# Kernel optimization log

Measured on AMD Instinct MI355X. Metric: run time of the kernel, lower is better.

The kernel has to match this reference:

```python
import jax, jax.numpy as jnp
import numpy as np

SR = 16000; HOP = 160; NM = 80; FMIN = 80.0; FMAX = 8000.0
T = 4 * SR              # 64000 samples
NSTAGE = 4              # cascaded biquad stages per channel
D = 256; NH = 8; DH = 32; NL = 8; DFF = 1024
BN_EPS = 1e-5; LN_EPS = 1e-5


def _biquad_coeffs():
    fc = np.logspace(np.log10(FMIN), np.log10(FMAX), NM)           # [NM]
    q = 4.0 + 2.0 * np.arange(NSTAGE)                               # [4]
    omega = 2.0 * np.pi * fc / SR
    alpha = np.sin(omega)[None, :] / (2.0 * q[:, None])             # [4,NM]
    a0 = 1.0 + alpha
    b0 = alpha / a0
    b2 = -alpha / a0
    a1 = (-2.0 * np.cos(omega))[None, :] / a0
    a2 = (1.0 - alpha) / a0
    return tuple(jnp.asarray(c, jnp.float32) for c in (b0, b2, a1, a2))


def _cochlear(x):
    # x: [B,T] -> [B,NM,T]; 4-stage cascaded bandpass biquads, zero initial state.
    b0, b2, a1, a2 = _biquad_coeffs()
    B = x.shape[0]
    z = jnp.zeros((NSTAGE, NM, B), x.dtype)

    def body(carry, xt):
        x1, x2, y1, y2 = carry                      # each [4,NM,B]
        sig = jnp.broadcast_to(xt[None, :], (NM, B))
        nx1, nx2, ny1, ny2 = [], [], [], []
        for s in range(NSTAGE):                     # fixed small cascade
            y = (b0[s][:, None] * sig + b2[s][:, None] * x2[s]
                 - a1[s][:, None] * y1[s] - a2[s][:, None] * y2[s])
            nx1.append(sig); nx2.append(x1[s]); ny1.append(y); ny2.append(y1[s])
            sig = y
        return (jnp.stack(nx1), jnp.stack(nx2), jnp.stack(ny1), jnp.stack(ny2)), sig

    _, ys = jax.lax.scan(body, (z, z, z, z), x.T)   # ys: [T,NM,B]
    return ys.transpose(2, 1, 0)


def _ln(x, g, b):
    m = x.mean(-1, keepdims=True)
    v = jnp.mean((x - m) ** 2, -1, keepdims=True)
    return (x - m) * jax.lax.rsqrt(v + LN_EPS) * g + b


def _cbr(h, w, b, g, bb):
    h = jax.lax.conv_general_dilated(h, w, (1, 1), 'SAME',
                                     dimension_numbers=('NCHW', 'OIHW', 'NCHW'))
    h = h + b[None, :, None, None]
    # eval-mode BatchNorm2d: running_mean=0, running_var=1
    h = h * (g / np.sqrt(1.0 + BN_EPS))[None, :, None, None] + bb[None, :, None, None]
    return jax.nn.relu(h)


def _mha(x, wqkv, bqkv, wo, bo):
    B, S, _ = x.shape
    qkv = x @ wqkv.T + bqkv
    q, k, v = jnp.split(qkv, 3, axis=-1)
    heads = lambda t: t.reshape(B, S, NH, DH).transpose(0, 2, 1, 3)
    q, k, v = heads(q), heads(k), heads(v)
    attn = jax.nn.softmax(jnp.einsum('bhqd,bhkd->bhqk', q, k) / np.sqrt(DH), axis=-1)
    o = jnp.einsum('bhqk,bhkd->bhqd', attn, v).transpose(0, 2, 1, 3).reshape(B, S, D)
    return o @ wo.T + bo


def _forward(x, cw1, cb1, g1, be1, cw2, cb2, g2, be2, cw3, cb3, g3, be3,
             qkv_w, qkv_b, out_w, out_b, ln1_g, ln1_b,
             ff1_w, ff1_b, ff2_w, ff2_b, ln2_g, ln2_b, pw, pb):
    B = x.shape[0]
    sig = _cochlear(x)                                    # [B,80,T]
    env = jnp.abs(sig)
    frames = env.reshape(B, NM, T // HOP, HOP).mean(-1)   # avg_pool1d k=s=160 -> [B,80,400]
    feats = jnp.log(frames + 1e-8)[:, None]               # [B,1,80,400]
    h = _cbr(feats, cw1, cb1, g1, be1)
    h = _cbr(h, cw2, cb2, g2, be2)
    h = _cbr(h, cw3, cb3, g3, be3)                        # [B,256,80,400]
    # AdaptiveAvgPool2d((80,32)): H already 80 (identity); pool W 400->32 with torch bin rule
    W_in, W_out = h.shape[-1], 32
    bins = [(int(np.floor(i * W_in / W_out)), int(np.ceil((i + 1) * W_in / W_out)))
            for i in range(W_out)]
    h = jnp.stack([h[..., s:e].mean(-1) for s, e in bins], axis=-1)   # [B,256,80,32]
    tok = h.reshape(B, D, -1).transpose(0, 2, 1)          # [B,2560,256]
    for l in range(NL):   # post-norm encoder layer, relu FFN, dropout=0 (eval)
        a = _mha(tok, qkv_w[l], qkv_b[l], out_w[l], out_b[l])
        tok = _ln(tok + a, ln1_g[l], ln1_b[l])
        f = jax.nn.relu(tok @ ff1_w[l].T + ff1_b[l]) @ ff2_w[l].T + ff2_b[l]
        tok = _ln(tok + f, ln2_g[l], ln2_b[l])
    return tok @ pw.T + pb                                # [B,2560,512]


def setup_inputs() -> dict:
    key = jax.random.key(0)
    ks = jax.random.split(key, 16)
    w = lambda k, shape, std=0.02: jax.random.normal(k, shape, jnp.float32) * std
    return {
        'x': jax.random.normal(ks[0], (1, T), jnp.float32),
        'cw1': w(ks[1], (64, 1, 3, 3), 0.1), 'cb1': jnp.zeros((64,)),
        'g1': jnp.ones((64,)), 'be1': jnp.zeros((64,)),
        'cw2': w(ks[2], (128, 64, 3, 3), 0.05), 'cb2': jnp.zeros((128,)),
        'g2': jnp.ones((128,)), 'be2': jnp.zeros((128,)),
        'cw3': w(ks[3], (256, 128, 3, 3), 0.05), 'cb3': jnp.zeros((256,)),
        'g3': jnp.ones((256,)), 'be3': jnp.zeros((256,)),
        'qkv_w': w(ks[4], (NL, 3 * D, D)), 'qkv_b': jnp.zeros((NL, 3 * D)),
        'out_w': w(ks[5], (NL, D, D)), 'out_b': jnp.zeros((NL, D)),
        'ln1_g': jnp.ones((NL, D)), 'ln1_b': jnp.zeros((NL, D)),
        'ff1_w': w(ks[6], (NL, DFF, D)), 'ff1_b': jnp.zeros((NL, DFF)),
        'ff2_w': w(ks[7], (NL, D, DFF)), 'ff2_b': jnp.zeros((NL, D)),
        'ln2_g': jnp.ones((NL, D)), 'ln2_b': jnp.zeros((NL, D)),
        'pw': w(ks[8], (512, D)), 'pb': jnp.zeros((512,)),
    }


def reference(x, cw1, cb1, g1, be1, cw2, cb2, g2, be2, cw3, cb3, g3, be3,
              qkv_w, qkv_b, out_w, out_b, ln1_g, ln1_b,
              ff1_w, ff1_b, ff2_w, ff2_b, ln2_g, ln2_b, pw, pb):
    return _forward(x, cw1, cb1, g1, be1, cw2, cb2, g2, be2, cw3, cb3, g3, be3,
                    qkv_w, qkv_b, out_w, out_b, ln1_g, ln1_b,
                    ff1_w, ff1_b, ff2_w, ff2_b, ln2_g, ln2_b, pw, pb)
```

## Files before the change

### kernel.cpp

```cpp
#include <hip/hip_runtime.h>
#include <hip/hip_bf16.h>
#include <math.h>

typedef __hip_bfloat16 bf16;
typedef short s16x8 __attribute__((ext_vector_type(8)));
typedef float f32x4 __attribute__((ext_vector_type(4)));

__device__ __forceinline__ float b2f(const bf16 v) { return __bfloat162float(v); }
__device__ __forceinline__ float ldf(int isbf, const void* p, size_t i) {
    return isbf ? __bfloat162float(((const bf16*)p)[i]) : ((const float*)p)[i];
}
__device__ __forceinline__ double ldd(int isbf, const void* p, size_t i) {
    return (double)ldf(isbf, p, i);
}
__device__ __forceinline__ short sbf(float f) {
    bf16 h = __float2bfloat16(f);
    return *(short*)&h;
}
__device__ __forceinline__ s16x8 cvt8(float4 a, float4 b) {
    union { bf16 h[8]; s16x8 v; } u;
    u.h[0] = __float2bfloat16(a.x); u.h[1] = __float2bfloat16(a.y);
    u.h[2] = __float2bfloat16(a.z); u.h[3] = __float2bfloat16(a.w);
    u.h[4] = __float2bfloat16(b.x); u.h[5] = __float2bfloat16(b.y);
    u.h[6] = __float2bfloat16(b.z); u.h[7] = __float2bfloat16(b.w);
    return u.v;
}

#define TLEN   64000
#define NMEL   80
#define CHUNK  160
#define NCHK   400
#define SEQ    2560
#define DMODEL 256
#define PI_D   3.14159265358979323846
#define CLW    420

#define F_COEF  0ul
#define F_FLAG  2560ul
#define F_M     2576ul
#define F_V     12816ul
#define F_INI   524816ul
#define F_FEATS 1036816ul
#define F_TOK   1068816ul
#define F_BIG   1724176ul
#define O_C1CL  0ul
#define O_C2CL  1102080ul
#define O_C3    3306240ul
#define O_WTB2  11500000ul
#define O_WTB3  11540000ul

__global__ void k_detect(const unsigned short* __restrict__ g, int* __restrict__ flag) {
    if (threadIdx.x == 0 && blockIdx.x == 0) *flag = (g[0] == 0x3F80) ? 1 : 0;
}

__global__ void k_coeffs(double* __restrict__ cf) {
    int i = blockIdx.x * 256 + threadIdx.x;
    if (i >= 4 * NMEL) return;
    int s = i / NMEL, m = i % NMEL;
    double lg0 = log10(80.0), lg1 = log10(8000.0);
    double fc = pow(10.0, lg0 + (lg1 - lg0) * (double)m / 79.0);
    double q = 4.0 + 2.0 * (double)s;
    double omega = 2.0 * PI_D * fc / 16000.0;
    double al = sin(omega) / (2.0 * q);
    double a0 = 1.0 + al;
    cf[i * 4 + 0] = (double)(float)(al / a0);
    cf[i * 4 + 1] = (double)(float)(-al / a0);
    cf[i * 4 + 2] = (double)(float)(-2.0 * cos(omega) / a0);
    cf[i * 4 + 3] = (double)(float)((1.0 - al) / a0);
}

__global__ __launch_bounds__(256) void k_bqf_zero(const void* __restrict__ x,
        const double* __restrict__ cf, const int* __restrict__ flagp,
        double* __restrict__ v) {
    int i = blockIdx.x * 256 + threadIdx.x;
    if (i >= NMEL * NCHK) return;
    int isbf = *flagp;
    int j = i / NMEL, m = i % NMEL;
    double b0[4], b2[4], a1[4], a2[4];
#pragma unroll
    for (int s = 0; s < 4; ++s) {
        const double* c = &cf[(s * NMEL + m) * 4];
        b0[s] = c[0]; b2[s] = c[1]; a1[s] = c[2]; a2[s] = c[3];
    }
    int t0 = j * CHUNK;
    double x1 = (t0 > 0) ? ldd(isbf, x, t0 - 1) : 0.0;
    double x2 = (t0 > 1) ? ldd(isbf, x, t0 - 2) : 0.0;
    double s0 = 0, s1 = 0, s2 = 0, s3 = 0, s4 = 0, s5 = 0, s6 = 0, s7 = 0;
    for (int t = t0; t < t0 + CHUNK; ++t) {
        double xt = ldd(isbf, x, t);
        double y0 = fma(b0[0], xt, fma(b2[0], x2, fma(-a1[0], s0, -a2[0] * s1)));
        double y1 = fma(b0[1], y0, fma(b2[1], s1, fma(-a1[1], s2, -a2[1] * s3)));
        double y2 = fma(b0[2], y1, fma(b2[2], s3, fma(-a1[2], s4, -a2[2] * s5)));
        double y3 = fma(b0[3], y2, fma(b2[3], s5, fma(-a1[3], s6, -a2[3] * s7)));
        s1 = s0; s0 = y0; s3 = s2; s2 = y1; s5 = s4; s4 = y2; s7 = s6; s6 = y3;
        x2 = x1; x1 = xt;
    }
    double* vp = &v[((size_t)m * NCHK + j) * 8];
    vp[0] = s0; vp[1] = s1; vp[2] = s2; vp[3] = s3;
    vp[4] = s4; vp[5] = s5; vp[6] = s6; vp[7] = s7;
}

__global__ __launch_bounds__(256) void k_bqA(const double* __restrict__ cf,
                                             double* __restrict__ M) {
    __shared__ double P[4][8][8], R[4][8][8], T[4][8][8];
    int t = threadIdx.x;
    int cg = t >> 6, e8 = t & 63;
    int i = e8 >> 3, jj = e8 & 7;
    int m = blockIdx.x * 4 + cg;
    double b0[4], b2[4], a1[4], a2[4];
#pragma unroll
    for (int s = 0; s < 4; ++s) {
        const double* c = &cf[(s * NMEL + m) * 4];
        b0[s] = c[0]; b2[s] = c[1]; a1[s] = c[2]; a2[s] = c[3];
    }
    double s[8];
#pragma unroll
    for (int k = 0; k < 8; ++k) s[k] = (k == jj) ? 1.0 : 0.0;
    double y0 = fma(-a1[0], s[0], -a2[0] * s[1]);
    double y1 = fma(b0[1], y0, fma(b2[1], s[1], fma(-a1[1], s[2], -a2[1] * s[3])));
    double y2 = fma(b0[2], y1, fma(b2[2], s[3], fma(-a1[2], s[4], -a2[2] * s[5])));
    double y3 = fma(b0[3], y2, fma(b2[3], s[5], fma(-a1[3], s[6], -a2[3] * s[7])));
    double colv[8] = {y0, s[0], y1, s[2], y2, s[4], y3, s[6]};
    P[cg][i][jj] = colv[i];
    R[cg][i][jj] = (i == jj) ? 1.0 : 0.0;
    __syncthreads();
    int e = CHUNK;
    while (e) {
        double acc = 0.0;
#pragma unroll
        for (int k = 0; k < 8; ++k) acc = fma(R[cg][i][k], P[cg][k][jj], acc);
        T[cg][i][jj] = acc;
        __syncthreads();
        if (e & 1) R[cg][i][jj] = T[cg][i][jj];
        __syncthreads();
        acc = 0.0;
#pragma unroll
        for (int k = 0; k < 8; ++k) acc = fma(P[cg][i][k], P[cg][k][jj], acc);
        T[cg][i][jj] = acc;
        __syncthreads();
        P[cg][i][jj] = T[cg][i][jj];
        e >>= 1;
        __syncthreads();
    }
    M[(size_t)m * 64 + i * 8 + jj] = R[cg][i][jj];
}

__global__ __launch_bounds__(512) void k_bq_scan8p(const double* __restrict__ Mbuf,
        const double* __restrict__ v, double* __restrict__ ini) {
    __shared__ double Mp[9][64];
    __shared__ double bufA[NCHK][8];
    __shared__ double bufB[NCHK][8];
    int m = blockIdx.x, t = threadIdx.x;
    if (t < 64) Mp[0][t] = Mbuf[(size_t)m * 64 + t];
    __syncthreads();
    for (int s = 1; s < 9; ++s) {
        if (t < 64) {
            int i = t >> 3, jj = t & 7;
            double acc = 0.0;
#pragma unroll
            for (int k = 0; k < 8; ++k) acc = fma(Mp[s - 1][i * 8 + k], Mp[s - 1][k * 8 + jj], acc);
            Mp[s][t] = acc;
        }
        __syncthreads();
    }
    double b[8];
    if (t < NCHK) {
        const double* vp = &v[((size_t)m * NCHK + t) * 8];
#pragma unroll
        for (int i = 0; i < 8; ++i) { b[i] = vp[i]; bufA[t][i] = b[i]; }
    }
    __syncthreads();
#pragma unroll
    for (int s = 0; s < 9; ++s) {
        int off = 1 << s;
        double nb[8];
        if (t < NCHK) {
            if (t >= off) {
                const double* src = (s & 1) ? bufB[t - off] : bufA[t - off];
#pragma unroll
                for (int i = 0; i < 8; ++i) {
                    double acc = b[i];
#pragma unroll
                    for (int k = 0; k < 8; ++k) acc = fma(Mp[s][i * 8 + k], src[k], acc);
                    nb[i] = acc;
                }
            } else {
#pragma unroll
                for (int i = 0; i < 8; ++i) nb[i] = b[i];
            }
        }
        __syncthreads();
        if (t < NCHK) {
            double* dst = (s & 1) ? bufA[t] : bufB[t];
#pragma unroll
            for (int i = 0; i < 8; ++i) { dst[i] = nb[i]; b[i] = nb[i]; }
        }
        __syncthreads();
    }
    if (t < NCHK) {
        double* op = &ini[((size_t)m * NCHK + t) * 8];
        if (t == 0) {
#pragma unroll
            for (int i = 0; i < 8; ++i) op[i] = 0.0;
        } else {
#pragma unroll
            for (int i = 0; i < 8; ++i) op[i] = bufB[t - 1][i];
        }
    }
}

__global__ __launch_bounds__(256) void k_bqf_emit(const void* __restrict__ x,
        const double* __restrict__ cf, const int* __restrict__ flagp,
        const double* __restrict__ ini, float* __restrict__ feats) {
    int i = blockIdx.x * 256 + threadIdx.x;
    if (i >= NMEL * NCHK) return;
    int isbf = *flagp;
    int j = i / NMEL, m = i % NMEL;
    double b0[4], b2[4], a1[4], a2[4];
#pragma unroll
    for (int s = 0; s < 4; ++s) {
        const double* c = &cf[(s * NMEL + m) * 4];
        b0[s] = c[0]; b2[s] = c[1]; a1[s] = c[2]; a2[s] = c[3];
    }
    int t0 = j * CHUNK;
    double x1 = (t0 > 0) ? ldd(isbf, x, t0 - 1) : 0.0;
    double x2 = (t0 > 1) ? ldd(isbf, x, t0 - 2) : 0.0;
    const double* ip = &ini[((size_t)m * NCHK + j) * 8];
    double s0 = ip[0], s1 = ip[1], s2 = ip[2], s3 = ip[3];
    double s4 = ip[4], s5 = ip[5], s6 = ip[6], s7 = ip[7];
    double acc = 0.0;
    for (int t = t0; t < t0 + CHUNK; ++t) {
        double xt = ldd(isbf, x, t);
        double y0 = fma(b0[0], xt, fma(b2[0], x2, fma(-a1[0], s0, -a2[0] * s1)));
        double y1 = fma(b0[1], y0, fma(b2[1], s1, fma(-a1[1], s2, -a2[1] * s3)));
        double y2 = fma(b0[2], y1, fma(b2[2], s3, fma(-a1[2], s4, -a2[2] * s5)));
        double y3 = fma(b0[3], y2, fma(b2[3], s5, fma(-a1[3], s6, -a2[3] * s7)));
        acc += fabs(y3);
        s1 = s0; s0 = y0; s3 = s2; s2 = y1; s5 = s4; s4 = y2; s7 = s6; s6 = y3;
        x2 = x1; x1 = xt;
    }
    feats[(size_t)m * 400 + j] = (float)log(acc * (1.0 / 160.0) + 1e-8);
}

__global__ void k_fill0(bf16* __restrict__ p, int n8) {
    int i = blockIdx.x * 256 + threadIdx.x;
    if (i < n8) { s16x8 z = {}; ((s16x8*)p)[i] = z; }
}

__global__ void k_wtb(const void* __restrict__ w, const int* __restrict__ flagp,
                      bf16* __restrict__ out, int CO, int CIN) {
    int i = blockIdx.x * 256 + threadIdx.x;
    int K = CIN * 9;
    if (i >= CO * K) return;
    int co = i / K, rem = i % K;
    int c = rem / 288, tp = (rem / 32) % 9, cin = rem & 31;
    out[i] = __float2bfloat16(ldf(*flagp, w, ((size_t)co * CIN + c * 32 + cin) * 9 + tp));
}

__global__ __launch_bounds__(256) void k_conv1cl(const float* __restrict__ in,
        const void* __restrict__ wt, const void* __restrict__ bi,
        const void* __restrict__ ga, const void* __restrict__ be,
        const int* __restrict__ flagp, bf16* __restrict__ out) {
    __shared__ float wsh[576];
    __shared__ float ash[64];
    __shared__ float bsh[64];
    int t = threadIdx.x;
    int isbf = *flagp;
    for (int i = t; i < 576; i += 256) wsh[i] = ldf(isbf, wt, i);
    if (t < 64) {
        float A = ldf(isbf, ga, t) * 0.999995000037f;
        ash[t] = A;
        bsh[t] = fmaf(ldf(isbf, bi, t), A, ldf(isbf, be, t));
    }
    __syncthreads();
    int i = blockIdx.x * 256 + t;
    if (i >= 32000) return;
    int h = i / 400, w = i % 400;
    float xs[9];
#pragma unroll
    for (int dy = 0; dy < 3; ++dy)
#pragma unroll
        for (int dx = 0; dx < 3; ++dx) {
            int hh = h + dy - 1, ww = w + dx - 1;
            xs[dy * 3 + dx] = (hh >= 0 && hh < 80 && ww >= 0 && ww < 400)
                              ? in[hh * 400 + ww] : 0.f;
        }
    bf16* op = out + ((size_t)(h + 1) * CLW + (w + 1)) * 64;
#pragma unroll
    for (int g = 0; g < 8; ++g) {
        union { bf16 h8[8]; s16x8 v; } u;
#pragma unroll
        for (int e = 0; e < 8; ++e) {
            int co = g * 8 + e;
            float acc = 0.f;
#pragma unroll
            for (int uu = 0; uu < 9; ++uu) acc = fmaf(wsh[co * 9 + uu], xs[uu], acc);
            u.h8[e] = __float2bfloat16(fmaxf(fmaf(acc, ash[co], bsh[co]), 0.f));
        }
        *(s16x8*)&op[g * 8] = u.v;
    }
}

template<int CIN, int CO, int CLOUT>
__global__ __launch_bounds__(256) void k_convm(const bf16* __restrict__ cl,
        const bf16* __restrict__ Wtb,
        const void* __restrict__ bi, const void* __restrict__ ga,
        const void* __restrict__ be, const int* __restrict__ flagp,
        void* __restrict__ out) {
    const int MT = CO / 64;
    const int K = CIN * 9;
    __shared__ short Bs[3][36][40];
    int t = threadIdx.x, wv = t >> 6, L = t & 63, quad = L >> 4, lx = L & 15;
    int w0 = blockIdx.x * 32, h = blockIdx.y;
    int cob = wv * (CO / 4);
    f32x4 acc[MT][2] = {};
    for (int c = 0; c < CIN / 32; ++c) {
        __syncthreads();
        for (int u = t; u < 408; u += 256) {
            int seg = u >> 2, part = u & 3;
            int dy = seg / 34, ww = seg % 34;
            *(s16x8*)&Bs[dy][ww][part * 8] =
                *(const s16x8*)&cl[((size_t)(h + dy) * CLW + (w0 + ww)) * CIN + c * 32 + part * 8];
        }
        __syncthreads();
#pragma unroll
        for (int tp = 0; tp < 9; ++tp) {
            int dy = tp / 3, dx = tp % 3;
            int kbase = (c * 9 + tp) * 32;
            s16x8 af[MT];
#pragma unroll
            for (int mt = 0; mt < MT; ++mt)
                af[mt] = *(const s16x8*)&Wtb[(size_t)(cob + mt * 16 + lx) * K + kbase + quad * 8];
#pragma unroll
            for (int n = 0; n < 2; ++n) {
                s16x8 bfr = *(const s16x8*)&Bs[dy][n * 16 + lx + dx][quad * 8];
#pragma unroll
                for (int mt = 0; mt < MT; ++mt)
                    acc[mt][n] = __builtin_amdgcn_mfma_f32_16x16x32_bf16(af[mt], bfr, acc[mt][n], 0, 0, 0);
            }
        }
    }
    int isbf = *flagp;
#pragma unroll
    for (int mt = 0; mt < MT; ++mt) {
#pragma unroll
        for (int r = 0; r < 4; ++r) {
            int co = cob + mt * 16 + quad * 4 + r;
            float A = ldf(isbf, ga, co) * 0.999995000037f;
            float B = fmaf(ldf(isbf, bi, co), A, ldf(isbf, be, co));
#pragma unroll
            for (int n = 0; n < 2; ++n) {
                int w = w0 + n * 16 + lx;
                if (w < 400) {
                    float v = fmaxf(fmaf(acc[mt][n][r], A, B), 0.f);
                    if (CLOUT)
                        ((bf16*)out)[((size_t)(h + 1) * CLW + (w + 1)) * CO + co] = __float2bfloat16(v);
                    else
                        ((float*)out)[(size_t)co * 32000 + h * 400 + w] = v;
                }
            }
        }
    }
}

__global__ __launch_bounds__(256) void k_pool(const float* __restrict__ c3,
                                              float* __restrict__ tok) {
    int i = blockIdx.x * 256 + threadIdx.x;
    if (i >= SEQ * DMODEL) return;
    int s = i >> 8, c = i & 255;
    int f = s >> 5, jj = s & 31;
    int w0 = (jj * 25) >> 1;
    const float* p = c3 + ((size_t)c * 80 + f) * 400 + w0;
    float sum = 0.f;
#pragma unroll
    for (int k = 0; k < 13; ++k) sum += p[k];
    tok[i] = sum * (1.f / 13.f);
}

template<int RELU, int OUTMODE, int NT, int ACOMB>
__global__ __launch_bounds__(256) void k_gemm(const float* __restrict__ A,
        const void* __restrict__ W, size_t woff,
        const void* __restrict__ bias, size_t boff,
        const int* __restrict__ flagp, void* __restrict__ Cout_,
        bf16* __restrict__ vtb, const float* __restrict__ partb,
        int M, int N, int K) {
    __shared__ short As[64][136];
    __shared__ short Bs[NT * 16][136];
    const int isbf = *flagp;
    int t = threadIdx.x;
    int wv = t >> 6, L = t & 63, quad = L >> 4, lx = L & 15;
    int row0 = blockIdx.y * 64, col0 = blockIdx.x * (NT * 16);
    f32x4 acc[NT] = {};
    for (int k0 = 0; k0 < K; k0 += 128) {
        __syncthreads();
        {
            int row = t >> 2, cb = (t & 3) * 8;
#pragma unroll
            for (int c = 0; c < 4; ++c) {
                int col = cb + c * 32;
                s16x8 av;
                if (ACOMB) {
                    int q = row0 + row;
                    int kk = k0 + col;
                    int hh = kk >> 5, d = kk & 31;
                    const float* pa = partb + ((size_t)(hh * 2) * SEQ + q) * 36;
                    const float* pc = pa + (size_t)SEQ * 36;
                    float m0 = pa[32], l0 = pa[33], m1 = pc[32], l1 = pc[33];
                    float Mx = fmaxf(m0, m1);
                    float e0 = __expf(m0 - Mx), e1 = __expf(m1 - Mx);
                    float inv = 1.f / (l0 * e0 + l1 * e1);
                    float4 u0 = *(const float4*)(pa + d), u1 = *(const float4*)(pa + d + 4);
                    float4 v0 = *(const float4*)(pc + d), v1 = *(const float4*)(pc + d + 4);
                    float4 r0, r1;
                    r0.x = (u0.x * e0 + v0.x * e1) * inv; r0.y = (u0.y * e0 + v0.y * e1) * inv;
                    r0.z = (u0.z * e0 + v0.z * e1) * inv; r0.w = (u0.w * e0 + v0.w * e1) * inv;
                    r1.x = (u1.x * e0 + v1.x * e1) * inv; r1.y = (u1.y * e0 + v1.y * e1) * inv;
                    r1.z = (u1.z * e0 + v1.z * e1) * inv; r1.w = (u1.w * e0 + v1.w * e1) * inv;
                    av = cvt8(r0, r1);
                } else {
                    const float* ap = &A[(size_t)(row0 + row) * K + k0 + col];
                    av = cvt8(*(const float4*)ap, *(const float4*)(ap + 4));
                }
                *(s16x8*)&As[row][col] = av;
            }
        }
        if (NT == 4) {
            int row = t >> 2, cb = (t & 3) * 8;
#pragma unroll
            for (int c = 0; c < 4; ++c) {
                int col = cb + c * 32;
                size_t widx = woff + (size_t)(col0 + row) * K + k0 + col;
                s16x8 wv8;
                if (isbf) {
                    wv8 = *(const s16x8*)((const bf16*)W + widx);
                } else {
                    const float* wf = (const float*)W + widx;
                    wv8 = cvt8(*(const float4*)wf, *(const float4*)(wf + 4));
                }
                *(s16x8*)&Bs[row][col] = wv8;
            }
        } else {
            int row = t >> 3, cb = (t & 7) * 8;
#pragma unroll
            for (int c = 0; c < 2; ++c) {
                int col = cb + c * 64;
                size_t widx = woff + (size_t)(col0 + row) * K + k0 + col;
                s16x8 wv8;
                if (isbf) {
                    wv8 = *(const s16x8*)((const bf16*)W + widx);
                } else {
                    const float* wf = (const float*)W + widx;
                    wv8 = cvt8(*(const float4*)wf, *(const float4*)(wf + 4));
                }
                *(s16x8*)&Bs[row][col] = wv8;
            }
        }
        __syncthreads();
#pragma unroll
        for (int kc = 0; kc < 4; ++kc) {
            s16x8 af = *(const s16x8*)&As[wv * 16 + lx][kc * 32 + quad * 8];
#pragma unroll
            for (int n = 0; n < NT; ++n) {
                s16x8 bf_ = *(const s16x8*)&Bs[n * 16 + lx][kc * 32 + quad * 8];
                acc[n] = __builtin_amdgcn_mfma_f32_16x16x32_bf16(af, bf_, acc[n], 0, 0, 0);
            }
        }
    }
#pragma unroll
    for (int n = 0; n < NT; ++n) {
        int col = col0 + n * 16 + lx;
        float bv = ldf(isbf, bias, boff + col);
#pragma unroll
        for (int r = 0; r < 4; ++r) {
            int row = row0 + wv * 16 + quad * 4 + r;
            float val = acc[n][r] + bv;
            if (RELU) val = fmaxf(val, 0.f);
            if (OUTMODE == 0) {
                ((float*)Cout_)[(size_t)row * N + col] = val;
            } else if (OUTMODE == 2) {
                bf16 bb_ = __float2bfloat16(val);
                ((bf16*)Cout_)[(size_t)row * N + col] = bb_;
                if (col >= 512) vtb[(size_t)(col - 512) * SEQ + row] = bb_;
            } else {
                if (isbf) ((bf16*)Cout_)[(size_t)row * N + col] = __float2bfloat16(val);
                else      ((float*)Cout_)[(size_t)row * N + col] = val;
            }
        }
    }
}

__global__ __launch_bounds__(256) void k_flash(const bf16* __restrict__ qkvB,
        const bf16* __restrict__ vtb, float* __restrict__ part) {
    int b = blockIdx.x;
    int pp = b & 1, qb = (b >> 1) % 40, h = b / 80;
    int t = threadIdx.x, wv = t >> 6, L = t & 63, quad = L >> 4, lx = L & 15;
    int q0 = qb * 64;
    __shared__ short Qs[64][40];
    __shared__ short Ks[64][40];
    __shared__ short Vt[32][72];
    __shared__ short Ps[64][72];
    const float scale = 0.17677669529663687f;
    int sr = t >> 2, sk = (t & 3) * 8;
    *(s16x8*)&Qs[sr][sk] = *(const s16x8*)&qkvB[(size_t)(q0 + sr) * 768 + h * 32 + sk];
    f32x4 o[2] = {};
    float mrow[4], lrow[4];
#pragma unroll
    for (int r = 0; r < 4; ++r) { mrow[r] = -INFINITY; lrow[r] = 0.f; }
    int kstart = pp * 1280;
    int vd = t >> 3, vk = (t & 7) * 8;
    for (int kt = 0; kt < 20; ++kt) {
        int kb = kstart + kt * 64;
        __syncthreads();
        *(s16x8*)&Ks[sr][sk] = *(const s16x8*)&qkvB[(size_t)(kb + sr) * 768 + 256 + h * 32 + sk];
        *(s16x8*)&Vt[vd][vk] = *(const s16x8*)&vtb[(size_t)(h * 32 + vd) * SEQ + kb + vk];
        __syncthreads();
        s16x8 qf = *(const s16x8*)&Qs[wv * 16 + lx][quad * 8];
        f32x4 sc[4] = {};
#pragma unroll
        for (int n = 0; n < 4; ++n) {
            s16x8 kf = *(const s16x8*)&Ks[n * 16 + lx][quad * 8];
            sc[n] = __builtin_amdgcn_mfma_f32_16x16x32_bf16(qf, kf, sc[n], 0, 0, 0);
        }
#pragma unroll
        for (int r = 0; r < 4; ++r) {
            float tm = -INFINITY;
#pragma unroll
            for (int n = 0; n < 4; ++n) { sc[n][r] *= scale; tm = fmaxf(tm, sc[n][r]); }
#pragma unroll
            for (int mk = 1; mk < 16; mk <<= 1) tm = fmaxf(tm, __shfl_xor(tm, mk));
            float mn = fmaxf(mrow[r], tm);
            float al = __expf(mrow[r] - mn);
            float ps = 0.f;
#pragma unroll
            for (int n = 0; n < 4; ++n) {
                float e = __expf(sc[n][r] - mn);
                sc[n][r] = e; ps += e;
            }
#pragma unroll
            for (int mk = 1; mk < 16; mk <<= 1) ps += __shfl_xor(ps, mk);
            lrow[r] = lrow[r] * al + ps;
            mrow[r] = mn;
            o[0][r] *= al; o[1][r] *= al;
            int qrow = wv * 16 + quad * 4 + r;
#pragma unroll
            for (int n = 0; n < 4; ++n) Ps[qrow][n * 16 + lx] = sbf(sc[n][r]);
        }
        __syncthreads();
#pragma unroll
        for (int ks = 0; ks < 2; ++ks) {
            s16x8 pf = *(const s16x8*)&Ps[wv * 16 + lx][ks * 32 + quad * 8];
#pragma unroll
            for (int n = 0; n < 2; ++n) {
                s16x8 vf = *(const s16x8*)&Vt[n * 16 + lx][ks * 32 + quad * 8];
                o[n] = __builtin_amdgcn_mfma_f32_16x16x32_bf16(pf, vf, o[n], 0, 0, 0);
            }
        }
    }
#pragma unroll
    for (int r = 0; r < 4; ++r) {
        int q = q0 + wv * 16 + quad * 4 + r;
        size_t pb_ = ((size_t)(h * 2 + pp) * SEQ + q) * 36;
        part[pb_ + lx] = o[0][r];
        part[pb_ + 16 + lx] = o[1][r];
        if (lx == 0) { part[pb_ + 32] = mrow[r]; part[pb_ + 33] = lrow[r]; }
    }
}

__global__ __launch_bounds__(256) void k_ln(float* __restrict__ tok,
        const float* __restrict__ res, const void* __restrict__ gg,
        const void* __restrict__ bb, size_t goff, const int* __restrict__ flagp) {
    int isbf = *flagp;
    int row = blockIdx.x * 4 + (threadIdx.x >> 6);
    int lane = threadIdx.x & 63;
    float* tp = tok + (size_t)row * DMODEL;
    const float* rp = res + (size_t)row * DMODEL;
    float4 a = *(const float4*)&tp[lane * 4];
    float4 r = *(const float4*)&rp[lane * 4];
    float x0 = a.x + r.x, x1 = a.y + r.y, x2 = a.z + r.z, x3 = a.w + r.w;
    float s = x0 + x1 + x2 + x3;
#pragma unroll
    for (int mk = 1; mk < 64; mk <<= 1) s += __shfl_xor(s, mk);
    float mean = s * (1.f / 256.f);
    float d0 = x0 - mean, d1 = x1 - mean, d2 = x2 - mean, d3 = x3 - mean;
    float vs = d0 * d0 + d1 * d1 + d2 * d2 + d3 * d3;
#pragma unroll
    for (int mk = 1; mk < 64; mk <<= 1) vs += __shfl_xor(vs, mk);
    float rstd = rsqrtf(vs * (1.f / 256.f) + 1e-5f);
    size_t c = goff + lane * 4;
    float y0 = fmaf(d0 * rstd, ldf(isbf, gg, c + 0), ldf(isbf, bb, c + 0));
    float y1 = fmaf(d1 * rstd, ldf(isbf, gg, c + 1), ldf(isbf, bb, c + 1));
    float y2 = fmaf(d2 * rstd, ldf(isbf, gg, c + 2), ldf(isbf, bb, c + 2));
    float y3 = fmaf(d3 * rstd, ldf(isbf, gg, c + 3), ldf(isbf, bb, c + 3));
    *(float4*)&tp[lane * 4] = make_float4(y0, y1, y2, y3);
}

extern "C" void kernel_launch(void* const* d_in, const int* in_sizes, int n_in,
                              void* d_out, int out_size, void* d_ws, size_t ws_size,
                              hipStream_t stream) {
    const void* x    = d_in[0];
    const void* cw1  = d_in[1];  const void* cb1 = d_in[2];
    const void* g1   = d_in[3];  const void* be1 = d_in[4];
    const void* cw2  = d_in[5];  const void* cb2 = d_in[6];
    const void* g2   = d_in[7];  const void* be2 = d_in[8];
    const void* cw3  = d_in[9];  const void* cb3 = d_in[10];
    const void* g3   = d_in[11]; const void* be3 = d_in[12];
    const void* qkvw = d_in[13]; const void* qkvb = d_in[14];
    const void* outw = d_in[15]; const void* outb = d_in[16];
    const void* ln1g = d_in[17]; const void* ln1b = d_in[18];
    const void* ff1w = d_in[19]; const void* ff1b = d_in[20];
    const void* ff2w = d_in[21]; const void* ff2b = d_in[22];
    const void* ln2g = d_in[23]; const void* ln2b = d_in[24];
    const void* pw   = d_in[25]; const void* pb   = d_in[26];

    float*  ws    = (float*)d_ws;
    double* coef  = (double*)(ws + F_COEF);
    int*    flagp = (int*)(ws + F_FLAG);
    double* Mbuf  = (double*)(ws + F_M);
    double* vbuf  = (double*)(ws + F_V);
    double* ini   = (double*)(ws + F_INI);
    float*  feats = ws + F_FEATS;
    float*  tok   = ws + F_TOK;
    bf16*   c1cl  = (bf16*)(ws + F_BIG + O_C1CL);
    bf16*   c2cl  = (bf16*)(ws + F_BIG + O_C2CL);
    float*  c3    = ws + F_BIG + O_C3;
    bf16*   Wtb2  = (bf16*)(ws + F_BIG + O_WTB2);
    bf16*   Wtb3  = (bf16*)(ws + F_BIG + O_WTB3);
    bf16*   qkvB  = (bf16*)(ws + F_BIG);
    bf16*   vtb   = (bf16*)(ws + F_BIG + 983040ul);
    float*  partb = ws + F_BIG + 1310720ul;
    float*  proj  = ws + F_BIG + 2785280ul;
    float*  ff1bf = ws + F_BIG + 3440640ul;

    k_detect<<<dim3(1), dim3(64), 0, stream>>>((const unsigned short*)ln1g, flagp);
    k_coeffs<<<dim3(2), dim3(256), 0, stream>>>(coef);
    k_wtb<<<dim3(288), dim3(256), 0, stream>>>(cw2, flagp, Wtb2, 128, 64);
    k_wtb<<<dim3(1152), dim3(256), 0, stream>>>(cw3, flagp, Wtb3, 256, 128);

    k_bqA<<<dim3(20), dim3(256), 0, stream>>>(coef, Mbuf);
    k_bqf_zero<<<dim3(125), dim3(256), 0, stream>>>(x, coef, flagp, vbuf);
    k_bq_scan8p<<<dim3(80), dim3(512), 0, stream>>>(Mbuf, vbuf, ini);
    k_bqf_emit<<<dim3(125), dim3(256), 0, stream>>>(x, coef, flagp, ini, feats);

    k_fill0<<<dim3(1077), dim3(256), 0, stream>>>(c1cl, 275520);
    k_fill0<<<dim3(2153), dim3(256), 0, stream>>>(c2cl, 551040);
    k_conv1cl<<<dim3(125), dim3(256), 0, stream>>>(feats, cw1, cb1, g1, be1, flagp, c1cl);
    k_convm<64, 128, 1><<<dim3(13, 80), dim3(256), 0, stream>>>(
        c1cl, Wtb2, cb2, g2, be2, flagp, c2cl);
    k_convm<128, 256, 0><<<dim3(13, 80), dim3(256), 0, stream>>>(
        c2cl, Wtb3, cb3, g3, be3, flagp, c3);

    k_pool<<<dim3(2560), dim3(256), 0, stream>>>(c3, tok);

    for (int l = 0; l < 8; ++l) {
        k_gemm<0, 2, 4, 0><<<dim3(12, 40), dim3(256), 0, stream>>>(
            tok, qkvw, (size_t)l * 768 * 256, qkvb, (size_t)l * 768,
            flagp, qkvB, vtb, nullptr, SEQ, 768, 256);
        k_flash<<<dim3(640), dim3(256), 0, stream>>>(qkvB, vtb, partb);
        k_gemm<0, 0, 2, 1><<<dim3(8, 40), dim3(256), 0, stream>>>(
            nullptr, outw, (size_t)l * 256 * 256, outb, (size_t)l * 256,
            flagp, proj, nullptr, partb, SEQ, 256, 256);
        k_ln<<<dim3(640), dim3(256), 0, stream>>>(tok, proj, ln1g, ln1b, (size_t)l * 256, flagp);
        k_gemm<1, 0, 4, 0><<<dim3(16, 40), dim3(256), 0, stream>>>(
            tok, ff1w, (size_t)l * 1024 * 256, ff1b, (size_t)l * 1024,
            flagp, ff1bf, nullptr, nullptr, SEQ, 1024, 256);
        k_gemm<0, 0, 2, 0><<<dim3(8, 40), dim3(256), 0, stream>>>(
            ff1bf, ff2w, (size_t)l * 256 * 1024, ff2b, (size_t)l * 256,
            flagp, proj, nullptr, nullptr, SEQ, 256, 1024);
        k_ln<<<dim3(640), dim3(256), 0, stream>>>(tok, proj, ln2g, ln2b, (size_t)l * 256, flagp);
    }

    k_gemm<0, 1, 2, 0><<<dim3(16, 40), dim3(256), 0, stream>>>(
        tok, pw, 0ul, pb, 0ul, flagp, d_out, nullptr, nullptr, SEQ, 512, 256);
}
```

Baseline: 1.273 ms.

## Fuse out-proj and FF2 GEMMs with residual LayerNorm; tile conv over two rows

Adds a full-row GEMM kernel (64 rows x 256 cols per block) that adds bias and residual and applies LayerNorm in the epilogue. It replaces the out-projection and FF2 GEMMs plus their separate LN kernels, which removes the proj round trip and two launches per layer. FF1 output now goes out as bf16 and FF2 reads it directly. The conv MFMA kernel also computes two output rows per block, reusing weight fragments and halving the grid. The trade-off is that the fused GEMM launches only 40 blocks, which may leave many CUs idle.

```diff
diff --git a/kernel.cpp b/kernel.cpp
--- a/kernel.cpp
+++ b/kernel.cpp
@@ -309,18 +309,18 @@
         void* __restrict__ out) {
     const int MT = CO / 64;
     const int K = CIN * 9;
-    __shared__ short Bs[3][36][40];
+    __shared__ short Bs[4][36][40];
     int t = threadIdx.x, wv = t >> 6, L = t & 63, quad = L >> 4, lx = L & 15;
-    int w0 = blockIdx.x * 32, h = blockIdx.y;
+    int w0 = blockIdx.x * 32, h0 = blockIdx.y * 2;
     int cob = wv * (CO / 4);
-    f32x4 acc[MT][2] = {};
+    f32x4 acc[MT][2][2] = {};
     for (int c = 0; c < CIN / 32; ++c) {
         __syncthreads();
-        for (int u = t; u < 408; u += 256) {
+        for (int u = t; u < 544; u += 256) {
             int seg = u >> 2, part = u & 3;
             int dy = seg / 34, ww = seg % 34;
             *(s16x8*)&Bs[dy][ww][part * 8] =
-                *(const s16x8*)&cl[((size_t)(h + dy) * CLW + (w0 + ww)) * CIN + c * 32 + part * 8];
+                *(const s16x8*)&cl[((size_t)(h0 + dy) * CLW + (w0 + ww)) * CIN + c * 32 + part * 8];
         }
         __syncthreads();
 #pragma unroll
@@ -332,11 +332,14 @@
             for (int mt = 0; mt < MT; ++mt)
                 af[mt] = *(const s16x8*)&Wtb[(size_t)(cob + mt * 16 + lx) * K + kbase + quad * 8];
 #pragma unroll
-            for (int n = 0; n < 2; ++n) {
-                s16x8 bfr = *(const s16x8*)&Bs[dy][n * 16 + lx + dx][quad * 8];
-#pragma unroll
-                for (int mt = 0; mt < MT; ++mt)
-                    acc[mt][n] = __builtin_amdgcn_mfma_f32_16x16x32_bf16(af[mt], bfr, acc[mt][n], 0, 0, 0);
+            for (int hr = 0; hr < 2; ++hr) {
+#pragma unroll
+                for (int n = 0; n < 2; ++n) {
+                    s16x8 bfr = *(const s16x8*)&Bs[dy + hr][n * 16 + lx + dx][quad * 8];
+#pragma unroll
+                    for (int mt = 0; mt < MT; ++mt)
+                        acc[mt][hr][n] = __builtin_amdgcn_mfma_f32_16x16x32_bf16(af[mt], bfr, acc[mt][hr][n], 0, 0, 0);
+                }
             }
         }
     }
@@ -349,14 +352,18 @@
             float A = ldf(isbf, ga, co) * 0.999995000037f;
             float B = fmaf(ldf(isbf, bi, co), A, ldf(isbf, be, co));
 #pragma unroll
-            for (int n = 0; n < 2; ++n) {
-                int w = w0 + n * 16 + lx;
-                if (w < 400) {
-                    float v = fmaxf(fmaf(acc[mt][n][r], A, B), 0.f);
-                    if (CLOUT)
-                        ((bf16*)out)[((size_t)(h + 1) * CLW + (w + 1)) * CO + co] = __float2bfloat16(v);
-                    else
-                        ((float*)out)[(size_t)co * 32000 + h * 400 + w] = v;
+            for (int hr = 0; hr < 2; ++hr) {
+                int h = h0 + hr;
+#pragma unroll
+                for (int n = 0; n < 2; ++n) {
+                    int w = w0 + n * 16 + lx;
+                    if (w < 400) {
+                        float v = fmaxf(fmaf(acc[mt][hr][n][r], A, B), 0.f);
+                        if (CLOUT)
+                            ((bf16*)out)[((size_t)(h + 1) * CLW + (w + 1)) * CO + co] = __float2bfloat16(v);
+                        else
+                            ((float*)out)[(size_t)co * 32000 + h * 400 + w] = v;
+                    }
                 }
             }
         }
@@ -481,10 +488,117 @@
                 bf16 bb_ = __float2bfloat16(val);
                 ((bf16*)Cout_)[(size_t)row * N + col] = bb_;
                 if (col >= 512) vtb[(size_t)(col - 512) * SEQ + row] = bb_;
+            } else if (OUTMODE == 3) {
+                ((bf16*)Cout_)[(size_t)row * N + col] = __float2bfloat16(val);
             } else {
                 if (isbf) ((bf16*)Cout_)[(size_t)row * N + col] = __float2bfloat16(val);
                 else      ((float*)Cout_)[(size_t)row * N + col] = val;
             }
+        }
+    }
+}
+
+template<int ABF16, int ACOMB>
+__global__ __launch_bounds__(256) void k_gemmln(const void* __restrict__ A,
+        const void* __restrict__ W, size_t woff,
+        const void* __restrict__ bias, size_t boff,
+        const void* __restrict__ gg, const void* __restrict__ bb, size_t goff,
+        const int* __restrict__ flagp, float* __restrict__ tok,
+        const float* __restrict__ partb, int K) {
+    __shared__ short As[64][72];
+    __shared__ short Bs[256][72];
+    const int isbf = *flagp;
+    int t = threadIdx.x;
+    int wv = t >> 6, L = t & 63, quad = L >> 4, lx = L & 15;
+    int row0 = blockIdx.x * 64;
+    f32x4 acc[16] = {};
+    for (int k0 = 0; k0 < K; k0 += 64) {
+        __syncthreads();
+        {
+            int row = t >> 2, cb = (t & 3) * 16;
+#pragma unroll
+            for (int c = 0; c < 2; ++c) {
+                int col = cb + c * 8;
+                s16x8 av;
+                if (ACOMB) {
+                    int q = row0 + row;
+                    int kk = k0 + col;
+                    int hh = kk >> 5, d = kk & 31;
+                    const float* pa = partb + ((size_t)(hh * 2) * SEQ + q) * 36;
+                    const float* pc = pa + (size_t)SEQ * 36;
+                    float m0 = pa[32], l0 = pa[33], m1 = pc[32], l1 = pc[33];
+                    float Mx = fmaxf(m0, m1);
+                    float e0 = __expf(m0 - Mx), e1 = __expf(m1 - Mx);
+                    float inv = 1.f / (l0 * e0 + l1 * e1);
+                    float4 u0 = *(const float4*)(pa + d), u1 = *(const float4*)(pa + d + 4);
+                    float4 v0 = *(const float4*)(pc + d), v1 = *(const float4*)(pc + d + 4);
+                    float4 r0, r1;
+                    r0.x = (u0.x * e0 + v0.x * e1) * inv; r0.y = (u0.y * e0 + v0.y * e1) * inv;
+                    r0.z = (u0.z * e0 + v0.z * e1) * inv; r0.w = (u0.w * e0 + v0.w * e1) * inv;
+                    r1.x = (u1.x * e0 + v1.x * e1) * inv; r1.y = (u1.y * e0 + v1.y * e1) * inv;
+                    r1.z = (u1.z * e0 + v1.z * e1) * inv; r1.w = (u1.w * e0 + v1.w * e1) * inv;
+                    av = cvt8(r0, r1);
+                } else if (ABF16) {
+                    av = *(const s16x8*)((const bf16*)A + (size_t)(row0 + row) * K + k0 + col);
+                } else {
+                    const float* ap = (const float*)A + (size_t)(row0 + row) * K + k0 + col;
+                    av = cvt8(*(const float4*)ap, *(const float4*)(ap + 4));
+                }
+                *(s16x8*)&As[row][col] = av;
+            }
+        }
+        {
+#pragma unroll
+            for (int c = 0; c < 8; ++c) {
+                int col = c * 8;
+                size_t widx = woff + (size_t)t * K + k0 + col;
+                s16x8 wv8;
+                if (isbf) {
+                    wv8 = *(const s16x8*)((const bf16*)W + widx);
+                } else {
+                    const float* wf = (const float*)W + widx;
+                    wv8 = cvt8(*(const float4*)wf, *(const float4*)(wf + 4));
+                }
+                *(s16x8*)&Bs[t][col] = wv8;
+            }
+        }
+        __syncthreads();
+#pragma unroll
+        for (int kc = 0; kc < 2; ++kc) {
+            s16x8 af = *(const s16x8*)&As[wv * 16 + lx][kc * 32 + quad * 8];
+#pragma unroll
+            for (int n = 0; n < 16; ++n) {
+                s16x8 bf_ = *(const s16x8*)&Bs[n * 16 + lx][kc * 32 + quad * 8];
+                acc[n] = __builtin_amdgcn_mfma_f32_16x16x32_bf16(af, bf_, acc[n], 0, 0, 0);
+            }
+        }
+    }
+#pragma unroll
+    for (int r = 0; r < 4; ++r) {
+        int row = row0 + wv * 16 + quad * 4 + r;
+        float* tp = tok + (size_t)row * DMODEL;
+        float vals[16];
+        float s = 0.f;
+#pragma unroll
+        for (int n = 0; n < 16; ++n) {
+            int col = n * 16 + lx;
+            float v = acc[n][r] + ldf(isbf, bias, boff + col) + tp[col];
+            vals[n] = v; s += v;
+        }
+#pragma unroll
+        for (int mk = 1; mk < 16; mk <<= 1) s += __shfl_xor(s, mk);
+        float mean = s * (1.f / 256.f);
+        float vs = 0.f;
+#pragma unroll
+        for (int n = 0; n < 16; ++n) { float d = vals[n] - mean; vs += d * d; }
+#pragma unroll
+        for (int mk = 1; mk < 16; mk <<= 1) vs += __shfl_xor(vs, mk);
+        float rstd = rsqrtf(vs * (1.f / 256.f) + 1e-5f);
+#pragma unroll
+        for (int n = 0; n < 16; ++n) {
+            int col = n * 16 + lx;
+            tp[col] = fmaf((vals[n] - mean) * rstd, ldf(isbf, gg, goff + col),
+                           ldf(isbf, bb, goff + col));
         }
     }
 }
@@ -564,34 +678,6 @@
         part[pb_ + 16 + lx] = o[1][r];
         if (lx == 0) { part[pb_ + 32] = mrow[r]; part[pb_ + 33] = lrow[r]; }
     }
-}
-
-__global__ __launch_bounds__(256) void k_ln(float* __restrict__ tok,
-        const float* __restrict__ res, const void* __restrict__ gg,
-        const void* __restrict__ bb, size_t goff, const int* __restrict__ flagp) {
-    int isbf = *flagp;
-    int row = blockIdx.x * 4 + (threadIdx.x >> 6);
-    int lane = threadIdx.x & 63;
-    float* tp = tok + (size_t)row * DMODEL;
-    const float* rp = res + (size_t)row * DMODEL;
-    float4 a = *(const float4*)&tp[lane * 4];
-    float4 r = *(const float4*)&rp[lane * 4];
-    float x0 = a.x + r.x, x1 = a.y + r.y, x2 = a.z + r.z, x3 = a.w + r.w;
-    float s = x0 + x1 + x2 + x3;
-#pragma unroll
-    for (int mk = 1; mk < 64; mk <<= 1) s += __shfl_xor(s, mk);
-    float mean = s * (1.f / 256.f);
-    float d0 = x0 - mean, d1 = x1 - mean, d2 = x2 - mean, d3 = x3 - mean;
-    float vs = d0 * d0 + d1 * d1 + d2 * d2 + d3 * d3;
-#pragma unroll
-    for (int mk = 1; mk < 64; mk <<= 1) vs += __shfl_xor(vs, mk);
-    float rstd = rsqrtf(vs * (1.f / 256.f) + 1e-5f);
-    size_t c = goff + lane * 4;
-    float y0 = fmaf(d0 * rstd, ldf(isbf, gg, c + 0), ldf(isbf, bb, c + 0));
-    float y1 = fmaf(d1 * rstd, ldf(isbf, gg, c + 1), ldf(isbf, bb, c + 1));
-    float y2 = fmaf(d2 * rstd, ldf(isbf, gg, c + 2), ldf(isbf, bb, c + 2));
-    float y3 = fmaf(d3 * rstd, ldf(isbf, gg, c + 3), ldf(isbf, bb, c + 3));
-    *(float4*)&tp[lane * 4] = make_float4(y0, y1, y2, y3);
 }
 
 extern "C" void kernel_launch(void* const* d_in, const int* in_sizes, int n_in,
@@ -628,8 +714,7 @@
     bf16*   qkvB  = (bf16*)(ws + F_BIG);
     bf16*   vtb   = (bf16*)(ws + F_BIG + 983040ul);
     float*  partb = ws + F_BIG + 1310720ul;
-    float*  proj  = ws + F_BIG + 2785280ul;
-    float*  ff1bf = ws + F_BIG + 3440640ul;
+    bf16*   ff1bf = (bf16*)(ws + F_BIG + 2785280ul);
 
     k_detect<<<dim3(1), dim3(64), 0, stream>>>((const unsigned short*)ln1g, flagp);
     k_coeffs<<<dim3(2), dim3(256), 0, stream>>>(coef);
@@ -644,9 +729,9 @@
     k_fill0<<<dim3(1077), dim3(256), 0, stream>>>(c1cl, 275520);
     k_fill0<<<dim3(2153), dim3(256), 0, stream>>>(c2cl, 551040);
     k_conv1cl<<<dim3(125), dim3(256), 0, stream>>>(feats, cw1, cb1, g1, be1, flagp, c1cl);
-    k_convm<64, 128, 1><<<dim3(13, 80), dim3(256), 0, stream>>>(
+    k_convm<64, 128, 1><<<dim3(13, 40), dim3(256), 0, stream>>>(
         c1cl, Wtb2, cb2, g2, be2, flagp, c2cl);
-    k_convm<128, 256, 0><<<dim3(13, 80), dim3(256), 0, stream>>>(
+    k_convm<128, 256, 0><<<dim3(13, 40), dim3(256), 0, stream>>>(
         c2cl, Wtb3, cb3, g3, be3, flagp, c3);
 
     k_pool<<<dim3(2560), dim3(256), 0, stream>>>(c3, tok);
@@ -656,17 +741,15 @@
             tok, qkvw, (size_t)l * 768 * 256, qkvb, (size_t)l * 768,
             flagp, qkvB, vtb, nullptr, SEQ, 768, 256);
         k_flash<<<dim3(640), dim3(256), 0, stream>>>(qkvB, vtb, partb);
-        k_gemm<0, 0, 2, 1><<<dim3(8, 40), dim3(256), 0, stream>>>(
+        k_gemmln<0, 1><<<dim3(40), dim3(256), 0, stream>>>(
             nullptr, outw, (size_t)l * 256 * 256, outb, (size_t)l * 256,
-            flagp, proj, nullptr, partb, SEQ, 256, 256);
-        k_ln<<<dim3(640), dim3(256), 0, stream>>>(tok, proj, ln1g, ln1b, (size_t)l * 256, flagp);
-        k_gemm<1, 0, 4, 0><<<dim3(16, 40), dim3(256), 0, stream>>>(
+            ln1g, ln1b, (size_t)l * 256, flagp, tok, partb, 256);
+        k_gemm<1, 3, 4, 0><<<dim3(16, 40), dim3(256), 0, stream>>>(
             tok, ff1w, (size_t)l * 1024 * 256, ff1b, (size_t)l * 1024,
             flagp, ff1bf, nullptr, nullptr, SEQ, 1024, 256);
-        k_gemm<0, 0, 2, 0><<<dim3(8, 40), dim3(256), 0, stream>>>(
+        k_gemmln<1, 0><<<dim3(40), dim3(256), 0, stream>>>(
             ff1bf, ff2w, (size_t)l * 256 * 1024, ff2b, (size_t)l * 256,
-            flagp, proj, nullptr, nullptr, SEQ, 256, 1024);
-        k_ln<<<dim3(640), dim3(256), 0, stream>>>(tok, proj, ln2g, ln2b, (size_t)l * 256, flagp);
+            ln2g, ln2b, (size_t)l * 256, flagp, tok, nullptr, 1024);
     }
 
     k_gemm<0, 1, 2, 0><<<dim3(16, 40), dim3(256), 0, stream>>>(
```

Result: slower. 1.768 ms (+38.9%).

## Compute two output rows per conv block and store FF1 activations as bf16

Applied to the files above, without the earlier changes.

The implicit-GEMM conv kernel now computes two output rows per block. It loads a 4-row halo into shared memory so each weight fragment feeds twice as many MFMAs, and the grid height is halved. Separately, the FF1 GEMM writes its ReLU output directly as bf16 and the FF2 GEMM reads bf16 activations without converting them. This halves that intermediate's traffic and removes the fp32-to-bf16 conversion. The cost is more accumulator registers and fewer blocks for the conv kernels.

```diff
diff --git a/kernel.cpp b/kernel.cpp
--- a/kernel.cpp
+++ b/kernel.cpp
@@ -309,18 +309,18 @@
         void* __restrict__ out) {
     const int MT = CO / 64;
     const int K = CIN * 9;
-    __shared__ short Bs[3][36][40];
+    __shared__ short Bs[4][36][40];
     int t = threadIdx.x, wv = t >> 6, L = t & 63, quad = L >> 4, lx = L & 15;
-    int w0 = blockIdx.x * 32, h = blockIdx.y;
+    int w0 = blockIdx.x * 32, h0 = blockIdx.y * 2;
     int cob = wv * (CO / 4);
-    f32x4 acc[MT][2] = {};
+    f32x4 acc[MT][2][2] = {};
     for (int c = 0; c < CIN / 32; ++c) {
         __syncthreads();
-        for (int u = t; u < 408; u += 256) {
+        for (int u = t; u < 544; u += 256) {
             int seg = u >> 2, part = u & 3;
             int dy = seg / 34, ww = seg % 34;
             *(s16x8*)&Bs[dy][ww][part * 8] =
-                *(const s16x8*)&cl[((size_t)(h + dy) * CLW + (w0 + ww)) * CIN + c * 32 + part * 8];
+                *(const s16x8*)&cl[((size_t)(h0 + dy) * CLW + (w0 + ww)) * CIN + c * 32 + part * 8];
         }
         __syncthreads();
 #pragma unroll
@@ -332,11 +332,14 @@
             for (int mt = 0; mt < MT; ++mt)
                 af[mt] = *(const s16x8*)&Wtb[(size_t)(cob + mt * 16 + lx) * K + kbase + quad * 8];
 #pragma unroll
-            for (int n = 0; n < 2; ++n) {
-                s16x8 bfr = *(const s16x8*)&Bs[dy][n * 16 + lx + dx][quad * 8];
-#pragma unroll
-                for (int mt = 0; mt < MT; ++mt)
-                    acc[mt][n] = __builtin_amdgcn_mfma_f32_16x16x32_bf16(af[mt], bfr, acc[mt][n], 0, 0, 0);
+            for (int hr = 0; hr < 2; ++hr) {
+#pragma unroll
+                for (int n = 0; n < 2; ++n) {
+                    s16x8 bfr = *(const s16x8*)&Bs[dy + hr][n * 16 + lx + dx][quad * 8];
+#pragma unroll
+                    for (int mt = 0; mt < MT; ++mt)
+                        acc[mt][hr][n] = __builtin_amdgcn_mfma_f32_16x16x32_bf16(af[mt], bfr, acc[mt][hr][n], 0, 0, 0);
+                }
             }
         }
     }
@@ -349,14 +352,18 @@
             float A = ldf(isbf, ga, co) * 0.999995000037f;
             float B = fmaf(ldf(isbf, bi, co), A, ldf(isbf, be, co));
 #pragma unroll
-            for (int n = 0; n < 2; ++n) {
-                int w = w0 + n * 16 + lx;
-                if (w < 400) {
-                    float v = fmaxf(fmaf(acc[mt][n][r], A, B), 0.f);
-                    if (CLOUT)
-                        ((bf16*)out)[((size_t)(h + 1) * CLW + (w + 1)) * CO + co] = __float2bfloat16(v);
-                    else
-                        ((float*)out)[(size_t)co * 32000 + h * 400 + w] = v;
+            for (int hr = 0; hr < 2; ++hr) {
+                int h = h0 + hr;
+#pragma unroll
+                for (int n = 0; n < 2; ++n) {
+                    int w = w0 + n * 16 + lx;
+                    if (w < 400) {
+                        float v = fmaxf(fmaf(acc[mt][hr][n][r], A, B), 0.f);
+                        if (CLOUT)
+                            ((bf16*)out)[((size_t)(h + 1) * CLW + (w + 1)) * CO + co] = __float2bfloat16(v);
+                        else
+                            ((float*)out)[(size_t)co * 32000 + h * 400 + w] = v;
+                    }
                 }
             }
         }
@@ -377,8 +384,8 @@
     tok[i] = sum * (1.f / 13.f);
 }
 
-template<int RELU, int OUTMODE, int NT, int ACOMB>
-__global__ __launch_bounds__(256) void k_gemm(const float* __restrict__ A,
+template<int RELU, int OUTMODE, int NT, int ACOMB, int ABF16>
+__global__ __launch_bounds__(256) void k_gemm(const void* __restrict__ A,
         const void* __restrict__ W, size_t woff,
         const void* __restrict__ bias, size_t boff,
         const int* __restrict__ flagp, void* __restrict__ Cout_,
@@ -417,8 +424,10 @@
                     r1.x = (u1.x * e0 + v1.x * e1) * inv; r1.y = (u1.y * e0 + v1.y * e1) * inv;
                     r1.z = (u1.z * e0 + v1.z * e1) * inv; r1.w = (u1.w * e0 + v1.w * e1) * inv;
                     av = cvt8(r0, r1);
+                } else if (ABF16) {
+                    av = *(const s16x8*)((const bf16*)A + (size_t)(row0 + row) * K + k0 + col);
                 } else {
-                    const float* ap = &A[(size_t)(row0 + row) * K + k0 + col];
+                    const float* ap = (const float*)A + (size_t)(row0 + row) * K + k0 + col;
                     av = cvt8(*(const float4*)ap, *(const float4*)(ap + 4));
                 }
                 *(s16x8*)&As[row][col] = av;
@@ -481,6 +490,8 @@
                 bf16 bb_ = __float2bfloat16(val);
                 ((bf16*)Cout_)[(size_t)row * N + col] = bb_;
                 if (col >= 512) vtb[(size_t)(col - 512) * SEQ + row] = bb_;
+            } else if (OUTMODE == 3) {
+                ((bf16*)Cout_)[(size_t)row * N + col] = __float2bfloat16(val);
             } else {
                 if (isbf) ((bf16*)Cout_)[(size_t)row * N + col] = __float2bfloat16(val);
                 else      ((float*)Cout_)[(size_t)row * N + col] = val;
@@ -629,7 +640,7 @@
     bf16*   vtb   = (bf16*)(ws + F_BIG + 983040ul);
     float*  partb = ws + F_BIG + 1310720ul;
     float*  proj  = ws + F_BIG + 2785280ul;
-    float*  ff1bf = ws + F_BIG + 3440640ul;
+    bf16*   ff1bf = (bf16*)(ws + F_BIG + 3440640ul);
 
     k_detect<<<dim3(1), dim3(64), 0, stream>>>((const unsigned short*)ln1g, flagp);
     k_coeffs<<<dim3(2), dim3(256), 0, stream>>>(coef);
@@ -644,31 +655,31 @@
     k_fill0<<<dim3(1077), dim3(256), 0, stream>>>(c1cl, 275520);
     k_fill0<<<dim3(2153), dim3(256), 0, stream>>>(c2cl, 551040);
     k_conv1cl<<<dim3(125), dim3(256), 0, stream>>>(feats, cw1, cb1, g1, be1, flagp, c1cl);
-    k_convm<64, 128, 1><<<dim3(13, 80), dim3(256), 0, stream>>>(
+    k_convm<64, 128, 1><<<dim3(13, 40), dim3(256), 0, stream>>>(
         c1cl, Wtb2, cb2, g2, be2, flagp, c2cl);
-    k_convm<128, 256, 0><<<dim3(13, 80), dim3(256), 0, stream>>>(
+    k_convm<128, 256, 0><<<dim3(13, 40), dim3(256), 0, stream>>>(
         c2cl, Wtb3, cb3, g3, be3, flagp, c3);
 
     k_pool<<<dim3(2560), dim3(256), 0, stream>>>(c3, tok);
 
     for (int l = 0; l < 8; ++l) {
-        k_gemm<0, 2, 4, 0><<<dim3(12, 40), dim3(256), 0, stream>>>(
+        k_gemm<0, 2, 4, 0, 0><<<dim3(12, 40), dim3(256), 0, stream>>>(
             tok, qkvw, (size_t)l * 768 * 256, qkvb, (size_t)l * 768,
             flagp, qkvB, vtb, nullptr, SEQ, 768, 256);
         k_flash<<<dim3(640), dim3(256), 0, stream>>>(qkvB, vtb, partb);
-        k_gemm<0, 0, 2, 1><<<dim3(8, 40), dim3(256), 0, stream>>>(
+        k_gemm<0, 0, 2, 1, 0><<<dim3(8, 40), dim3(256), 0, stream>>>(
             nullptr, outw, (size_t)l * 256 * 256, outb, (size_t)l * 256,
             flagp, proj, nullptr, partb, SEQ, 256, 256);
         k_ln<<<dim3(640), dim3(256), 0, stream>>>(tok, proj, ln1g, ln1b, (size_t)l * 256, flagp);
-        k_gemm<1, 0, 4, 0><<<dim3(16, 40), dim3(256), 0, stream>>>(
+        k_gemm<1, 3, 4, 0, 0><<<dim3(16, 40), dim3(256), 0, stream>>>(
             tok, ff1w, (size_t)l * 1024 * 256, ff1b, (size_t)l * 1024,
             flagp, ff1bf, nullptr, nullptr, SEQ, 1024, 256);
-        k_gemm<0, 0, 2, 0><<<dim3(8, 40), dim3(256), 0, stream>>>(
+        k_gemm<0, 0, 2, 0, 1><<<dim3(8, 40), dim3(256), 0, stream>>>(
             ff1bf, ff2w, (size_t)l * 256 * 1024, ff2b, (size_t)l * 256,
             flagp, proj, nullptr, nullptr, SEQ, 256, 1024);
         k_ln<<<dim3(640), dim3(256), 0, stream>>>(tok, proj, ln2g, ln2b, (size_t)l * 256, flagp);
     }
 
-    k_gemm<0, 1, 2, 0><<<dim3(16, 40), dim3(256), 0, stream>>>(
+    k_gemm<0, 1, 2, 0, 0><<<dim3(16, 40), dim3(256), 0, stream>>>(
         tok, pw, 0ul, pb, 0ul, flagp, d_out, nullptr, nullptr, SEQ, 512, 256);
 }
```

After: 1.194 ms. 6.3% less time.
